# Optimization experiments

Measured on AMD Instinct MI355X. Metric: run time of the kernel, lower is better.

The kernel has to match this reference:

```python
import jax, jax.numpy as jnp
import numpy as np
from itertools import product

D = 128        # input voxel grid side
N_IN = 150000  # active input voxels
C_IN = 32
C_OUT = 64
M = 100000     # active output voxels kept after stride-2 downsample
EPS = 1e-5


def _build_rulebooks():
    rng = np.random.default_rng(0)
    flat = rng.choice(D ** 3, size=N_IN, replace=False)
    coords = np.stack(np.unravel_index(flat, (D, D, D)), axis=1).astype(np.int64)  # [N_IN,3]
    # SparseConv3d(kernel=2, stride=2, padding=1): input i contributes to output o with
    # i = 2*o - 1 + k, k in {0,1}; per dim exactly one k is valid -> o = (i+1)//2.
    out_all = (coords + 1) // 2
    koff = (coords + 1) % 2
    kidx = koff[:, 0] * 4 + koff[:, 1] * 2 + koff[:, 2]
    out_coords, inv = np.unique(out_all, axis=0, return_inverse=True)
    assert len(out_coords) >= M, 'not enough occupied parent voxels'
    out_coords = out_coords[:M]
    nbr_down = -np.ones((M, 8), np.int32)
    sel = inv < M
    nbr_down[inv[sel], kidx[sel]] = np.arange(N_IN, dtype=np.int32)[sel]
    # SubMConv3d(kernel=3, padding=1): output sites == input sites; neighbor table per offset.
    S = 67  # hash stride (out coords in [0,65), +1 shift keeps neighbor keys in range)
    key = (out_coords[:, 0] + 1) * S * S + (out_coords[:, 1] + 1) * S + (out_coords[:, 2] + 1)
    lut = -np.ones(S ** 3, np.int32)
    lut[key] = np.arange(M, dtype=np.int32)
    nbr_sub = np.empty((M, 27), np.int32)
    for k, (dx, dy, dz) in enumerate(product((-1, 0, 1), repeat=3)):
        nbr_sub[:, k] = lut[key + dx * S * S + dy * S + dz]
    return nbr_down, nbr_sub


def setup_inputs() -> dict:
    nbr_down, nbr_sub = _build_rulebooks()
    key = jax.random.key(0)
    k0, k1, k2, k3, k4 = jax.random.split(key, 5)
    ones = jnp.ones((C_OUT,), jnp.float32)
    zeros = jnp.zeros((C_OUT,), jnp.float32)
    return {
        'x_feats': jax.random.normal(k0, (N_IN, C_IN), jnp.float32),
        'w_down': jax.random.normal(k1, (8, C_IN, C_OUT), jnp.float32) / np.sqrt(8 * C_IN),
        'g_down': ones, 'b_down': zeros,
        'w_proj': jax.random.normal(k2, (C_OUT, C_OUT), jnp.float32) / np.sqrt(C_OUT),
        'g_p': ones, 'b_p': zeros,
        'w1': jax.random.normal(k3, (27, C_OUT, C_OUT), jnp.float32) / np.sqrt(27 * C_OUT),
        'g1': ones, 'b1': zeros,
        'w2': jax.random.normal(k4, (27, C_OUT, C_OUT), jnp.float32) / np.sqrt(27 * C_OUT),
        'g2': ones, 'b2': zeros,
        'nbr_down': jnp.asarray(nbr_down),
        'nbr_sub': jnp.asarray(nbr_sub),
    }


def _bn(f, g, b):
    # BatchNorm1d in training mode over the active-voxel dim (biased variance)
    m = f.mean(0)
    v = jnp.mean((f - m) ** 2, 0)
    return (f - m) * jax.lax.rsqrt(v + EPS) * g + b


def _spconv(feats, nbr, W):
    # rulebook gather-GEMM-scatter: out[m] = sum_k feats[nbr[m,k]] @ W[k]  (nbr=-1 -> zero)
    n = feats.shape[0]
    fpad = jnp.concatenate([feats, jnp.zeros((1, feats.shape[1]), feats.dtype)], axis=0)
    idx = jnp.where(nbr < 0, n, nbr)
    out = jnp.zeros((nbr.shape[0], W.shape[2]), feats.dtype)
    for k in range(W.shape[0]):  # fixed small kernel volume (8 or 27)
        out = out + fpad[idx[:, k]] @ W[k]
    return out


def reference(x_feats, w_down, g_down, b_down, w_proj, g_p, b_p,
              w1, g1, b1, w2, g2, b2, nbr_down, nbr_sub):
    # DonwBlock.down: SparseConv3d -> BN -> ReLU
    x = jax.nn.relu(_bn(_spconv(x_feats, nbr_down, w_down), g_down, b_down))
    # DoubleConv.proj: 1x1 SubMConv (plain linear on features) -> BN
    res = _bn(x @ w_proj, g_p, b_p)
    # conv1 -> bn1 -> relu -> conv2 -> bn2 -> +proj -> relu
    out = jax.nn.relu(_bn(_spconv(x, nbr_sub, w1), g1, b1))
    out = _bn(_spconv(out, nbr_sub, w2), g2, b2) + res
    return jax.nn.relu(out)
```

## Files before the change

kernel.cpp:

```cpp
#include <hip/hip_runtime.h>

static constexpr int M_ROWS = 100000;
static constexpr int N_IN   = 150000;
static constexpr int C_IN   = 32;
static constexpr int CO     = 64;
static constexpr float EPS  = 1e-5f;

typedef __bf16 bf16x8 __attribute__((ext_vector_type(8)));
typedef float  f32x4  __attribute__((ext_vector_type(4)));
typedef unsigned short u16x8 __attribute__((ext_vector_type(8)));
typedef short  short8 __attribute__((ext_vector_type(8)));
typedef unsigned int u32;

static __device__ __forceinline__ unsigned short f2bf(float f) {
    unsigned int u = __builtin_bit_cast(unsigned int, f);
    u += 0x7fff + ((u >> 16) & 1);
    return (unsigned short)(u >> 16);
}
static __device__ __forceinline__ float bf2f(unsigned short h) {
    unsigned int u = ((unsigned int)h) << 16;
    return __builtin_bit_cast(float, u);
}

static __device__ __forceinline__ void gload_lds16(const void* g, void* l) {
    __builtin_amdgcn_global_load_lds(
        (const __attribute__((address_space(1))) u32*)g,
        (__attribute__((address_space(3))) u32*)l, 16, 0, 0);
}

__global__ __launch_bounds__(256) void cvt_bf16(
    const float* __restrict__ in, unsigned short* __restrict__ out, int n8)
{
    int i = blockIdx.x * 256 + threadIdx.x;
    if (i >= n8) return;
    float4 a = ((const float4*)in)[2 * i];
    float4 b = ((const float4*)in)[2 * i + 1];
    u16x8 v;
    v[0] = f2bf(a.x); v[1] = f2bf(a.y); v[2] = f2bf(a.z); v[3] = f2bf(a.w);
    v[4] = f2bf(b.x); v[5] = f2bf(b.y); v[6] = f2bf(b.z); v[7] = f2bf(b.w);
    ((u16x8*)out)[i] = v;
}

__global__ __launch_bounds__(256) void wt_cvt_swz(
    const float* __restrict__ W, unsigned short* __restrict__ WT, int total, int cin)
{
    int t = blockIdx.x * 256 + threadIdx.x;
    if (t >= total) return;
    int k  = t / (cin * 64);
    int r  = t - k * (cin * 64);
    int ci = r >> 6;
    int co = r & 63;
    int xm = (cin == 64) ? ((co & 7) << 4) : ((co & 3) << 4);
    int phys = co * (cin * 2) + ((ci * 2) ^ xm);
    WT[(size_t)k * cin * 64 + (phys >> 1)] = f2bf(W[t]);
}

template<int CIN, int KOFF, int PH, bool GATHER, bool OUTBF>
__global__ __launch_bounds__(256, 2) void spconv_mfma(
    const unsigned short* __restrict__ fB,
    int nZero,
    const int*   __restrict__ nbr,
    const unsigned short* __restrict__ WTs,
    void* __restrict__ outp,
    float* __restrict__ part)
{
    constexpr int KS    = CIN / 32;
    constexpr int ST    = 2;
    constexpr int SLAB  = CIN * 64;
    constexpr int P1    = (KOFF < PH) ? KOFF : PH;
    constexpr int NF    = KOFF / PH;
    constexpr int T     = KOFF - NF * PH;

    __shared__ unsigned short Wl[P1 * SLAB];
    __shared__ int nbrS[GATHER ? 128 * KOFF : 4];
    __shared__ float red[4][2][64];

    const int tid  = threadIdx.x;
    const int lane = tid & 63;
    const int wv   = tid >> 6;
    const int colb = lane & 15;
    const int kgrp = lane >> 4;

    const int nwg = gridDim.x;
    const int q   = nwg >> 3, r8 = nwg & 7;
    const int xcd = blockIdx.x & 7, pos = blockIdx.x >> 3;
    const int wg  = (xcd < r8 ? xcd * (q + 1) : r8 * (q + 1) + (xcd - r8) * q) + pos;
    const int m0  = wg * 128;

    auto stageN = [&](int k0, int cnt) {
        const unsigned short* g = WTs + (size_t)k0 * SLAB;
        const int reps = cnt * (SLAB / 2048);
        for (int r = 0; r < reps; ++r) {
            const void* gp = g + (size_t)(r * 256 + tid) * 8;
            void* lp = &Wl[(size_t)(r * 256 + wv * 64) * 8];
            gload_lds16(gp, lp);
        }
    };

    stageN(0, P1);
    if (GATHER) {
        const int* src = nbr + (size_t)m0 * KOFF;
        constexpr int TOT = 128 * KOFF;
        if (m0 + 128 <= M_ROWS) {
            #pragma unroll 1
            for (int i = tid; i < TOT / 4; i += 256)
                ((int4*)nbrS)[i] = ((const int4*)src)[i];
        } else {
            #pragma unroll 1
            for (int i = tid; i < TOT; i += 256) {
                int r = i / KOFF;
                nbrS[i] = (m0 + r < M_ROWS) ? src[i] : -1;
            }
        }
    }
    __syncthreads();

    auto gatherA = [&](int k, bf16x8 (&dst)[ST][KS]) {
        #pragma unroll
        for (int st = 0; st < ST; ++st) {
            int rloc = wv * (ST * 16) + st * 16 + colb;
            int idx;
            if (GATHER) idx = nbrS[rloc * KOFF + k];
            else        idx = (m0 + rloc < M_ROWS) ? (m0 + rloc) : -1;
            if (idx < 0) idx = nZero;
            const unsigned short* fp = fB + (size_t)idx * CIN + kgrp * 8;
            #pragma unroll
            for (int s = 0; s < KS; ++s)
                dst[st][s] = *reinterpret_cast<const bf16x8*>(fp + s * 32);
        }
    };

    f32x4 acc[ST][4] = {};

    auto compute = [&](int slab, const bf16x8 (&a)[ST][KS]) {
        bf16x8 w[4][KS];
        const char* base = (const char*)&Wl[0] + (size_t)slab * SLAB * 2;
        #pragma unroll
        for (int n = 0; n < 4; ++n) {
            int r  = n * 16 + colb;
            int xm = (CIN == 64) ? ((r & 7) << 4) : ((r & 3) << 4);
            #pragma unroll
            for (int s = 0; s < KS; ++s) {
                int c2 = kgrp * 16 + s * 64;
                int phys = r * (CIN * 2) + (c2 ^ xm);
                w[n][s] = *reinterpret_cast<const bf16x8*>(base + phys);
            }
        }
        #pragma unroll
        for (int st = 0; st < ST; ++st)
            #pragma unroll
            for (int n = 0; n < 4; ++n)
                #pragma unroll
                for (int s = 0; s < KS; ++s)
                    acc[st][n] = __builtin_amdgcn_mfma_f32_16x16x32_bf16(
                        a[st][s], w[n][s], acc[st][n], 0, 0, 0);
    };

    #pragma unroll 1
    for (int p = 0; p < NF; ++p) {
        const int k0 = p * PH;
        #pragma unroll
        for (int kk = 0; kk < PH; ++kk) {
            bf16x8 a[ST][KS];
            gatherA(k0 + kk, a);
            compute(kk, a);
        }
        if (p + 1 < NF || T > 0) {
            __syncthreads();
            stageN((p + 1) * PH, (p + 1 < NF) ? PH : T);
            __syncthreads();
        }
    }
    if (T > 0) {
        #pragma unroll
        for (int kk = 0; kk < T; ++kk) {
            bf16x8 a[ST][KS];
            gatherA(NF * PH + kk, a);
            compute(kk, a);
        }
    }

    #pragma unroll
    for (int st = 0; st < ST; ++st) {
        int rbase = m0 + wv * (ST * 16) + st * 16 + kgrp * 4;
        #pragma unroll
        for (int j = 0; j < 4; ++j) {
            int row = rbase + j;
            if (row < M_ROWS) {
                if (OUTBF) {
                    unsigned short* o = (unsigned short*)outp;
                    #pragma unroll
                    for (int n = 0; n < 4; ++n)
                        o[(size_t)row * 64 + n * 16 + colb] = f2bf(acc[st][n][j]);
                } else {
                    float* o = (float*)outp;
                    #pragma unroll
                    for (int n = 0; n < 4; ++n)
                        o[(size_t)row * 64 + n * 16 + colb] = acc[st][n][j];
                }
            }
        }
    }

    float s4[4], q4[4];
    #pragma unroll
    for (int n = 0; n < 4; ++n) {
        float s = 0.f, qq = 0.f;
        #pragma unroll
        for (int st = 0; st < ST; ++st)
            #pragma unroll
            for (int j = 0; j < 4; ++j) {
                float v = acc[st][n][j];
                s += v; qq += v * v;
            }
        s4[n] = s; q4[n] = qq;
    }
    #pragma unroll
    for (int n = 0; n < 4; ++n) {
        s4[n] += __shfl_xor(s4[n], 16); s4[n] += __shfl_xor(s4[n], 32);
        q4[n] += __shfl_xor(q4[n], 16); q4[n] += __shfl_xor(q4[n], 32);
    }
    if (kgrp == 0) {
        #pragma unroll
        for (int n = 0; n < 4; ++n) {
            red[wv][0][n * 16 + colb] = s4[n];
            red[wv][1][n * 16 + colb] = q4[n];
        }
    }
    __syncthreads();
    if (tid < 64) {
        float S = red[0][0][tid] + red[1][0][tid] + red[2][0][tid] + red[3][0][tid];
        float Q = red[0][1][tid] + red[1][1][tid] + red[2][1][tid] + red[3][1][tid];
        part[(size_t)wg * 128 + tid]      = S;
        part[(size_t)wg * 128 + 64 + tid] = Q;
    }
}

__global__ __launch_bounds__(1024) void bn_finalize(
    const float* __restrict__ part, int nblocks,
    const float* __restrict__ gg, const float* __restrict__ bb,
    float* __restrict__ ss, int M)
{
    const int tid = threadIdx.x;
    const int c   = tid & 63;
    const int grp = tid >> 6;
    float S = 0.f, Q = 0.f;
    int i = grp;
    for (; i + 48 < nblocks; i += 64) {
        float a0 = part[(size_t)(i     ) * 128 + c];
        float a1 = part[(size_t)(i + 16) * 128 + c];
        float a2 = part[(size_t)(i + 32) * 128 + c];
        float a3 = part[(size_t)(i + 48) * 128 + c];
        float q0 = part[(size_t)(i     ) * 128 + 64 + c];
        float q1 = part[(size_t)(i + 16) * 128 + 64 + c];
        float q2 = part[(size_t)(i + 32) * 128 + 64 + c];
        float q3 = part[(size_t)(i + 48) * 128 + 64 + c];
        S += a0 + a1 + a2 + a3;
        Q += q0 + q1 + q2 + q3;
    }
    for (; i < nblocks; i += 16) {
        S += part[(size_t)i * 128 + c];
        Q += part[(size_t)i * 128 + 64 + c];
    }
    __shared__ float sh[2][16][64];
    sh[0][grp][c] = S; sh[1][grp][c] = Q;
    __syncthreads();
    if (tid < 64) {
        float Sa = 0.f, Qa = 0.f;
        #pragma unroll
        for (int j = 0; j < 16; ++j) { Sa += sh[0][j][tid]; Qa += sh[1][j][tid]; }
        float mean = Sa / (float)M;
        float var  = Qa / (float)M - mean * mean;
        float rstd = rsqrtf(var + EPS);
        float sc = gg[tid] * rstd;
        ss[tid]      = sc;
        ss[64 + tid] = bb[tid] - mean * sc;
    }
}

template<bool INBF, bool BF16OUT, bool RES, bool RELU>
__global__ __launch_bounds__(256) void bn_apply(
    const void* __restrict__ yp, const float* __restrict__ ss,
    const unsigned short* __restrict__ res, void* __restrict__ out, int n8)
{
    for (int i = blockIdx.x * 256 + threadIdx.x; i < n8; i += gridDim.x * 256) {
        float v[8];
        if (INBF) {
            u16x8 u = ((const u16x8*)yp)[i];
            #pragma unroll
            for (int j = 0; j < 8; ++j) v[j] = bf2f(u[j]);
        } else {
            float4 a = ((const float4*)yp)[2 * i];
            float4 b = ((const float4*)yp)[2 * i + 1];
            v[0] = a.x; v[1] = a.y; v[2] = a.z; v[3] = a.w;
            v[4] = b.x; v[5] = b.y; v[6] = b.z; v[7] = b.w;
        }
        int c0 = (i * 8) & 63;
        #pragma unroll
        for (int j = 0; j < 8; ++j)
            v[j] = v[j] * ss[c0 + j] + ss[64 + c0 + j];
        if (RES) {
            u16x8 rv = ((const u16x8*)res)[i];
            #pragma unroll
            for (int j = 0; j < 8; ++j) v[j] += bf2f(rv[j]);
        }
        if (RELU) {
            #pragma unroll
            for (int j = 0; j < 8; ++j) v[j] = fmaxf(v[j], 0.f);
        }
        if (BF16OUT) {
            u16x8 o;
            #pragma unroll
            for (int j = 0; j < 8; ++j) o[j] = f2bf(v[j]);
            ((u16x8*)out)[i] = o;
        } else {
            float4 oa, ob;
            oa.x = v[0]; oa.y = v[1]; oa.z = v[2]; oa.w = v[3];
            ob.x = v[4]; ob.y = v[5]; ob.z = v[6]; ob.w = v[7];
            ((float4*)out)[2 * i]     = oa;
            ((float4*)out)[2 * i + 1] = ob;
        }
    }
}

extern "C" void kernel_launch(void* const* d_in, const int* in_sizes, int n_in,
                              void* d_out, int out_size, void* d_ws, size_t ws_size,
                              hipStream_t stream)
{
    const float* x_feats = (const float*)d_in[0];
    const float* w_down  = (const float*)d_in[1];
    const float* g_down  = (const float*)d_in[2];
    const float* b_down  = (const float*)d_in[3];
    const float* w_proj  = (const float*)d_in[4];
    const float* g_p     = (const float*)d_in[5];
    const float* b_p     = (const float*)d_in[6];
    const float* w1      = (const float*)d_in[7];
    const float* g1      = (const float*)d_in[8];
    const float* b1      = (const float*)d_in[9];
    const float* w2      = (const float*)d_in[10];
    const float* g2      = (const float*)d_in[11];
    const float* b2      = (const float*)d_in[12];
    const int*   nbr_down = (const int*)d_in[13];
    const int*   nbr_sub  = (const int*)d_in[14];
    float* out = (float*)d_out;

    const int M = M_ROWS;
    const int conv_grid = (M + 127) / 128;
    const size_t feat4 = (size_t)M * CO * 4;
    const size_t feat2 = (size_t)(M + 1) * CO * 2;
    auto align = [](size_t x) { return (x + 255) & ~(size_t)255; };

    char* ws = (char*)d_ws;
    size_t off = 0;
    unsigned short* xin16 = (unsigned short*)(ws + off); off += align((size_t)(N_IN + 1) * C_IN * 2);
    unsigned short* wdT   = (unsigned short*)(ws + off); off += align((size_t)8 * CO * C_IN * 2);
    unsigned short* wpT   = (unsigned short*)(ws + off); off += align((size_t)1 * CO * CO * 2);
    unsigned short* w1T   = (unsigned short*)(ws + off); off += align((size_t)27 * CO * CO * 2);
    unsigned short* w2T   = (unsigned short*)(ws + off); off += align((size_t)27 * CO * CO * 2);
    float* Y    = (float*)(ws + off); off += align(feat4);
    unsigned short* bufRb = (unsigned short*)(ws + off); off += align(feat2);
    unsigned short* xB = (unsigned short*)(ws + off); off += align(feat2);
    unsigned short* zB = (unsigned short*)(ws + off); off += align(feat2);
    float* part = (float*)(ws + off); off += align((size_t)1024 * 128 * 4);
    float* ss0  = (float*)(ws + off);
    float* ss1  = ss0 + 128;
    float* ss2  = ss1 + 128;
    float* ss3  = ss2 + 128;

    unsigned short* Yb = (unsigned short*)Y;

    const int n8 = M * CO / 8;
    const int ew_grid = 2048;

    hipMemsetAsync(xin16 + (size_t)N_IN * C_IN, 0, C_IN * 2, stream);
    hipMemsetAsync(xB + (size_t)M * CO, 0, CO * 2, stream);
    hipMemsetAsync(zB + (size_t)M * CO, 0, CO * 2, stream);

    {
        int nf8 = N_IN * C_IN / 8;
        cvt_bf16<<<(nf8 + 255) / 256, 256, 0, stream>>>(x_feats, xin16, nf8);
        int t;
        t = 8 * C_IN * CO;  wt_cvt_swz<<<(t + 255) / 256, 256, 0, stream>>>(w_down, wdT, t, C_IN);
        t = CO * CO;        wt_cvt_swz<<<(t + 255) / 256, 256, 0, stream>>>(w_proj, wpT, t, CO);
        t = 27 * CO * CO;   wt_cvt_swz<<<(t + 255) / 256, 256, 0, stream>>>(w1, w1T, t, CO);
        t = 27 * CO * CO;   wt_cvt_swz<<<(t + 255) / 256, 256, 0, stream>>>(w2, w2T, t, CO);
    }

    spconv_mfma<C_IN, 8, 8, true, true><<<conv_grid, 256, 0, stream>>>(
        xin16, N_IN, nbr_down, wdT, Yb, part);
    bn_finalize<<<1, 1024, 0, stream>>>(part, conv_grid, g_down, b_down, ss0, M);
    bn_apply<true, true, false, true><<<ew_grid, 256, 0, stream>>>(Yb, ss0, nullptr, xB, n8);

    spconv_mfma<CO, 1, 1, false, true><<<conv_grid, 256, 0, stream>>>(
        xB, M, nullptr, wpT, Yb, part);
    bn_finalize<<<1, 1024, 0, stream>>>(part, conv_grid, g_p, b_p, ss1, M);
    bn_apply<true, true, false, false><<<ew_grid, 256, 0, stream>>>(Yb, ss1, nullptr, bufRb, n8);

    spconv_mfma<CO, 27, 8, true, true><<<conv_grid, 256, 0, stream>>>(
        xB, M, nbr_sub, w1T, Yb, part);
    bn_finalize<<<1, 1024, 0, stream>>>(part, conv_grid, g1, b1, ss2, M);
    bn_apply<true, true, false, true><<<ew_grid, 256, 0, stream>>>(Yb, ss2, nullptr, zB, n8);

    spconv_mfma<CO, 27, 8, true, false><<<conv_grid, 256, 0, stream>>>(
        zB, M, nbr_sub, w2T, Y, part);
    bn_finalize<<<1, 1024, 0, stream>>>(part, conv_grid, g2, b2, ss3, M);
    bn_apply<false, false, true, true><<<ew_grid, 256, 0, stream>>>(Y, ss3, bufRb, out, n8);
}
```

Measured before the change: 196.6 us.

## Stage contiguous neighbor feature windows in LDS for 27-tap submanifold convs

Adds a dedicated 27-tap submanifold conv kernel. For each group of three taps (a fixed dx,dy pair) it computes the minimum neighbor index and stages a contiguous window of FCAP feature rows, plus that group's three weight slabs, into double-buffered LDS. Taps whose neighbor falls inside the window read from LDS, the rest fall back to global loads. Feature buffers are written XOR-swizzled by bn_apply to avoid LDS bank conflicts and are padded with FCAP zero rows so the window never overreads. This trades a large LDS footprint and extra branching for less repeated global gather traffic, relying on the spatial locality of sorted coordinates.

```diff
diff --git a/kernel.cpp b/kernel.cpp
--- a/kernel.cpp
+++ b/kernel.cpp
@@ -5,6 +5,7 @@
 static constexpr int C_IN   = 32;
 static constexpr int CO     = 64;
 static constexpr float EPS  = 1e-5f;
+static constexpr int  FCAP  = 256;
 
 typedef __bf16 bf16x8 __attribute__((ext_vector_type(8)));
 typedef float  f32x4  __attribute__((ext_vector_type(4)));
@@ -20,6 +21,10 @@
 static __device__ __forceinline__ float bf2f(unsigned short h) {
     unsigned int u = ((unsigned int)h) << 16;
     return __builtin_bit_cast(float, u);
+}
+static __device__ __forceinline__ bf16x8 bfzero() {
+    short8 z = {0,0,0,0,0,0,0,0};
+    return __builtin_bit_cast(bf16x8, z);
 }
 
 static __device__ __forceinline__ void gload_lds16(const void* g, void* l) {
@@ -55,7 +60,7 @@
     WT[(size_t)k * cin * 64 + (phys >> 1)] = f2bf(W[t]);
 }
 
-template<int CIN, int KOFF, int PH, bool GATHER, bool OUTBF>
+template<int CIN, int KOFF, int PH, bool GATHER, bool OUTBF, bool SWZIN>
 __global__ __launch_bounds__(256, 2) void spconv_mfma(
     const unsigned short* __restrict__ fB,
     int nZero,
@@ -123,10 +128,12 @@
             if (GATHER) idx = nbrS[rloc * KOFF + k];
             else        idx = (m0 + rloc < M_ROWS) ? (m0 + rloc) : -1;
             if (idx < 0) idx = nZero;
-            const unsigned short* fp = fB + (size_t)idx * CIN + kgrp * 8;
+            const char* gb = (const char*)(fB + (size_t)idx * CIN);
+            int xm = SWZIN ? ((idx & 7) << 4) : 0;
             #pragma unroll
             for (int s = 0; s < KS; ++s)
-                dst[st][s] = *reinterpret_cast<const bf16x8*>(fp + s * 32);
+                dst[st][s] = *reinterpret_cast<const bf16x8*>(
+                    gb + ((kgrp * 16 + s * 64) ^ xm));
         }
     };
 
@@ -208,6 +215,193 @@
         float s = 0.f, qq = 0.f;
         #pragma unroll
         for (int st = 0; st < ST; ++st)
+            #pragma unroll
+            for (int j = 0; j < 4; ++j) {
+                float v = acc[st][n][j];
+                s += v; qq += v * v;
+            }
+        s4[n] = s; q4[n] = qq;
+    }
+    #pragma unroll
+    for (int n = 0; n < 4; ++n) {
+        s4[n] += __shfl_xor(s4[n], 16); s4[n] += __shfl_xor(s4[n], 32);
+        q4[n] += __shfl_xor(q4[n], 16); q4[n] += __shfl_xor(q4[n], 32);
+    }
+    if (kgrp == 0) {
+        #pragma unroll
+        for (int n = 0; n < 4; ++n) {
+            red[wv][0][n * 16 + colb] = s4[n];
+            red[wv][1][n * 16 + colb] = q4[n];
+        }
+    }
+    __syncthreads();
+    if (tid < 64) {
+        float S = red[0][0][tid] + red[1][0][tid] + red[2][0][tid] + red[3][0][tid];
+        float Q = red[0][1][tid] + red[1][1][tid] + red[2][1][tid] + red[3][1][tid];
+        part[(size_t)wg * 128 + tid]      = S;
+        part[(size_t)wg * 128 + 64 + tid] = Q;
+    }
+}
+
+template<bool OUTBF>
+__global__ __launch_bounds__(256) void spconv_sub27(
+    const unsigned short* __restrict__ fBs,
+    const int*   __restrict__ nbr,
+    const unsigned short* __restrict__ WTs,
+    void* __restrict__ outp,
+    float* __restrict__ part)
+{
+    constexpr int SLAB = 64 * 64;
+
+    __shared__ unsigned short featL[2][FCAP * 64];
+    __shared__ unsigned short Wl[2][3 * SLAB];
+    __shared__ int   nbrS[128 * 27];
+    __shared__ int   loS[9];
+    __shared__ float red[4][2][64];
+
+    const int tid  = threadIdx.x;
+    const int lane = tid & 63;
+    const int wv   = tid >> 6;
+    const int colb = lane & 15;
+    const int kgrp = lane >> 4;
+
+    const int nwg = gridDim.x;
+    const int q   = nwg >> 3, r8 = nwg & 7;
+    const int xcd = blockIdx.x & 7, pos = blockIdx.x >> 3;
+    const int wg  = (xcd < r8 ? xcd * (q + 1) : r8 * (q + 1) + (xcd - r8) * q) + pos;
+    const int m0  = wg * 128;
+
+    {
+        const int* src = nbr + (size_t)m0 * 27;
+        if (m0 + 128 <= M_ROWS) {
+            #pragma unroll 1
+            for (int i = tid; i < 864; i += 256)
+                ((int4*)nbrS)[i] = ((const int4*)src)[i];
+        } else {
+            #pragma unroll 1
+            for (int i = tid; i < 3456; i += 256) {
+                int r = i / 27;
+                nbrS[i] = (m0 + r < M_ROWS) ? src[i] : -1;
+            }
+        }
+        if (tid < 9) loS[tid] = 0x7fffffff;
+    }
+    __syncthreads();
+    #pragma unroll 1
+    for (int i = tid; i < 3456; i += 256) {
+        int v = nbrS[i];
+        if (v >= 0) atomicMin(&loS[(i % 27) / 3], v);
+    }
+    __syncthreads();
+
+    auto stageF = [&](int g, int b) {
+        int lg = loS[g]; if (lg == 0x7fffffff) lg = 0;
+        const unsigned short* gp0 = fBs + (size_t)lg * 64;
+        #pragma unroll
+        for (int r = 0; r < 8; ++r) {
+            const void* gp = gp0 + (size_t)(r * 256 + tid) * 8;
+            void* lp = &featL[b][(size_t)(r * 256 + wv * 64) * 8];
+            gload_lds16(gp, lp);
+        }
+    };
+    auto stageWg = [&](int g, int b) {
+        const unsigned short* gp0 = WTs + (size_t)(3 * g) * SLAB;
+        #pragma unroll
+        for (int r = 0; r < 6; ++r) {
+            const void* gp = gp0 + (size_t)(r * 256 + tid) * 8;
+            void* lp = &Wl[b][(size_t)(r * 256 + wv * 64) * 8];
+            gload_lds16(gp, lp);
+        }
+    };
+
+    f32x4 acc[2][4] = {};
+
+    auto dotap = [&](int k, int slab, int b, int lg) {
+        bf16x8 a[2][2];
+        #pragma unroll
+        for (int st = 0; st < 2; ++st) {
+            int rloc = wv * 32 + st * 16 + colb;
+            int idx = nbrS[rloc * 27 + k];
+            if (idx < 0) {
+                a[st][0] = bfzero(); a[st][1] = bfzero();
+            } else {
+                int xm = (idx & 7) << 4;
+                unsigned off = (unsigned)(idx - lg);
+                if (off < (unsigned)FCAP) {
+                    const char* base = (const char*)&featL[b][0] + (size_t)off * 128;
+                    a[st][0] = *(const bf16x8*)(base + ((kgrp * 16 +  0) ^ xm));
+                    a[st][1] = *(const bf16x8*)(base + ((kgrp * 16 + 64) ^ xm));
+                } else {
+                    const char* gb = (const char*)(fBs + (size_t)idx * 64);
+                    a[st][0] = *(const bf16x8*)(gb + ((kgrp * 16 +  0) ^ xm));
+                    a[st][1] = *(const bf16x8*)(gb + ((kgrp * 16 + 64) ^ xm));
+                }
+            }
+        }
+        bf16x8 w[4][2];
+        const char* wbase = (const char*)&Wl[b][0] + (size_t)slab * SLAB * 2;
+        #pragma unroll
+        for (int n = 0; n < 4; ++n) {
+            int r  = n * 16 + colb;
+            int xm = (r & 7) << 4;
+            #pragma unroll
+            for (int s = 0; s < 2; ++s) {
+                int phys = r * 128 + ((kgrp * 16 + s * 64) ^ xm);
+                w[n][s] = *reinterpret_cast<const bf16x8*>(wbase + phys);
+            }
+        }
+        #pragma unroll
+        for (int st = 0; st < 2; ++st)
+            #pragma unroll
+            for (int n = 0; n < 4; ++n)
+                #pragma unroll
+                for (int s = 0; s < 2; ++s)
+                    acc[st][n] = __builtin_amdgcn_mfma_f32_16x16x32_bf16(
+                        a[st][s], w[n][s], acc[st][n], 0, 0, 0);
+    };
+
+    stageF(0, 0); stageWg(0, 0);
+    __syncthreads();
+
+    int buf = 0;
+    #pragma unroll 1
+    for (int g = 0; g < 9; ++g) {
+        if (g + 1 < 9) { stageF(g + 1, buf ^ 1); stageWg(g + 1, buf ^ 1); }
+        int lg = loS[g]; if (lg == 0x7fffffff) lg = 0;
+        #pragma unroll
+        for (int t3 = 0; t3 < 3; ++t3) dotap(3 * g + t3, t3, buf, lg);
+        if (g + 1 < 9) __syncthreads();
+        buf ^= 1;
+    }
+
+    #pragma unroll
+    for (int st = 0; st < 2; ++st) {
+        int rbase = m0 + wv * 32 + st * 16 + kgrp * 4;
+        #pragma unroll
+        for (int j = 0; j < 4; ++j) {
+            int row = rbase + j;
+            if (row < M_ROWS) {
+                if (OUTBF) {
+                    unsigned short* o = (unsigned short*)outp;
+                    #pragma unroll
+                    for (int n = 0; n < 4; ++n)
+                        o[(size_t)row * 64 + n * 16 + colb] = f2bf(acc[st][n][j]);
+                } else {
+                    float* o = (float*)outp;
+                    #pragma unroll
+                    for (int n = 0; n < 4; ++n)
+                        o[(size_t)row * 64 + n * 16 + colb] = acc[st][n][j];
+                }
+            }
+        }
+    }
+
+    float s4[4], q4[4];
+    #pragma unroll
+    for (int n = 0; n < 4; ++n) {
+        float s = 0.f, qq = 0.f;
+        #pragma unroll
+        for (int st = 0; st < 2; ++st)
             #pragma unroll
             for (int j = 0; j < 4; ++j) {
                 float v = acc[st][n][j];
@@ -278,7 +472,7 @@
     }
 }
 
-template<bool INBF, bool BF16OUT, bool RES, bool RELU>
+template<bool INBF, bool BF16OUT, bool RES, bool RELU, bool OUTSWZ>
 __global__ __launch_bounds__(256) void bn_apply(
     const void* __restrict__ yp, const float* __restrict__ ss,
     const unsigned short* __restrict__ res, void* __restrict__ out, int n8)
@@ -312,7 +506,9 @@
             u16x8 o;
             #pragma unroll
             for (int j = 0; j < 8; ++j) o[j] = f2bf(v[j]);
-            ((u16x8*)out)[i] = o;
+            int oi = i;
+            if (OUTSWZ) oi = (i & ~7) | ((i & 7) ^ ((i >> 3) & 7));
+            ((u16x8*)out)[oi] = o;
         } else {
             float4 oa, ob;
             oa.x = v[0]; oa.y = v[1]; oa.z = v[2]; oa.w = v[3];
@@ -347,7 +543,7 @@
     const int M = M_ROWS;
     const int conv_grid = (M + 127) / 128;
     const size_t feat4 = (size_t)M * CO * 4;
-    const size_t feat2 = (size_t)(M + 1) * CO * 2;
+    const size_t feat2 = (size_t)(M + 1 + FCAP) * CO * 2;
     auto align = [](size_t x) { return (x + 255) & ~(size_t)255; };
 
     char* ws = (char*)d_ws;
@@ -373,8 +569,8 @@
     const int ew_grid = 2048;
 
     hipMemsetAsync(xin16 + (size_t)N_IN * C_IN, 0, C_IN * 2, stream);
-    hipMemsetAsync(xB + (size_t)M * CO, 0, CO * 2, stream);
-    hipMemsetAsync(zB + (size_t)M * CO, 0, CO * 2, stream);
+    hipMemsetAsync(xB + (size_t)M * CO, 0, (1 + FCAP) * CO * 2, stream);
+    hipMemsetAsync(zB + (size_t)M * CO, 0, (1 + FCAP) * CO * 2, stream);
 
     {
         int nf8 = N_IN * C_IN / 8;
@@ -386,23 +582,21 @@
         t = 27 * CO * CO;   wt_cvt_swz<<<(t + 255) / 256, 256, 0, stream>>>(w2, w2T, t, CO);
     }
 
-    spconv_mfma<C_IN, 8, 8, true, true><<<conv_grid, 256, 0, stream>>>(
+    spconv_mfma<C_IN, 8, 8, true, true, false><<<conv_grid, 256, 0, stream>>>(
         xin16, N_IN, nbr_down, wdT, Yb, part);
     bn_finalize<<<1, 1024, 0, stream>>>(part, conv_grid, g_down, b_down, ss0, M);
-    bn_apply<true, true, false, true><<<ew_grid, 256, 0, stream>>>(Yb, ss0, nullptr, xB, n8);
-
-    spconv_mfma<CO, 1, 1, false, true><<<conv_grid, 256, 0, stream>>>(
+    bn_apply<true, true, false, true, true><<<ew_grid, 256, 0, stream>>>(Yb, ss0, nullptr, xB, n8);
+
+    spconv_mfma<CO, 1, 1, false, true, true><<<conv_grid, 256, 0, stream>>>(
         xB, M, nullptr, wpT, Yb, part);
     bn_finalize<<<1, 1024, 0, stream>>>(part, conv_grid, g_p, b_p, ss1, M);
-    bn_apply<true, true, false, false><<<ew_grid, 256, 0, stream>>>(Yb, ss1, nullptr, bufRb, n8);
-
-    spconv_mfma<CO, 27, 8, true, true><<<conv_grid, 256, 0, stream>>>(
-        xB, M, nbr_sub, w1T, Yb, part);
+    bn_apply<true, true, false, false, false><<<ew_grid, 256, 0, stream>>>(Yb, ss1, nullptr, bufRb, n8);
+
+    spconv_sub27<true><<<conv_grid, 256, 0, stream>>>(xB, nbr_sub, w1T, Yb, part);
     bn_finalize<<<1, 1024, 0, stream>>>(part, conv_grid, g1, b1, ss2, M);
-    bn_apply<true, true, false, true><<<ew_grid, 256, 0, stream>>>(Yb, ss2, nullptr, zB, n8);
-
-    spconv_mfma<CO, 27, 8, true, false><<<conv_grid, 256, 0, stream>>>(
-        zB, M, nbr_sub, w2T, Y, part);
+    bn_apply<true, true, false, true, true><<<ew_grid, 256, 0, stream>>>(Yb, ss2, nullptr, zB, n8);
+
+    spconv_sub27<false><<<conv_grid, 256, 0, stream>>>(zB, nbr_sub, w2T, Y, part);
     bn_finalize<<<1, 1024, 0, stream>>>(part, conv_grid, g2, b2, ss3, M);
-    bn_apply<false, false, true, true><<<ew_grid, 256, 0, stream>>>(Y, ss3, bufRb, out, n8);
-}
+    bn_apply<false, false, true, true, false><<<ew_grid, 256, 0, stream>>>(Y, ss3, bufRb, out, n8);
+}
```

Measured after the change: 254.1 us. +29.2%, slower.
